# Performance work log

Hardware: AMD Instinct MI355X
Metric: run time of the kernel (lower is better)

## Reference

```python
import jax, jax.numpy as jnp
import numpy as np

N = 50000      # total nodes
NPG = 1000     # nodes per graph
B = 50         # graphs in batch
E = 800000     # positive edges
HID = 64
LN_EPS = 1e-5


def setup_inputs() -> dict:
    key = jax.random.key(0)
    ks = jax.random.split(key, 8)
    h = jax.random.normal(ks[0], (N, HID), jnp.float32)
    W1 = jax.random.normal(ks[1], (HID + 1, 2 * HID), jnp.float32) * 0.1
    b1 = jnp.zeros((2 * HID,), jnp.float32)
    ln_g = jnp.ones((2 * HID,), jnp.float32)
    ln_b = jnp.zeros((2 * HID,), jnp.float32)
    W2 = jax.random.normal(ks[2], (2 * HID, 1), jnp.float32) * 0.1
    b2 = jnp.zeros((1,), jnp.float32)
    # positive edges: endpoints within the same graph (contiguous node blocks)
    src_p = jax.random.randint(ks[3], (E,), 0, N)
    dst_p = (src_p // NPG) * NPG + jax.random.randint(ks[4], (E,), 0, NPG)
    pos_edge = jnp.stack([src_p, dst_p]).astype(jnp.int32)
    # negative edges: same-graph random pairs (stand-in for batched_negative_sampling)
    src_n = jax.random.randint(ks[5], (E,), 0, N)
    dst_n = (src_n // NPG) * NPG + jax.random.randint(ks[6], (E,), 0, NPG)
    neg_edge = jnp.stack([src_n, dst_n]).astype(jnp.int32)
    node_batch = jnp.arange(N, dtype=jnp.int32) // NPG
    return {"h": h, "W1": W1, "b1": b1, "ln_g": ln_g, "ln_b": ln_b,
            "W2": W2, "b2": b2, "pos_edge": pos_edge, "neg_edge": neg_edge,
            "node_batch": node_batch, "num_graphs": B}


def reference(h, W1, b1, ln_g, ln_b, W2, b2, pos_edge, neg_edge, node_batch, num_graphs):
    Epos = pos_edge.shape[1]
    T = 2 * Epos
    nb = int(num_graphs)
    # concat pos+neg edges, stable sort by graph id of source node
    edges_all = jnp.concatenate([pos_edge, neg_edge], axis=1)      # [2, T]
    idx = jnp.argsort(node_batch[edges_all[0]])                    # stable
    edges = edges_all[:, idx]
    conn = (idx < Epos).astype(h.dtype)                            # 1 = positive edge
    # pair features + connectivity flag -> tiny MLP score
    enc = jnp.concatenate([h[edges[0]] + h[edges[1]], conn[:, None]], axis=-1)  # [T, HID+1]
    x = enc @ W1 + b1                                              # [T, 2*HID]
    mu = jnp.mean(x, axis=-1, keepdims=True)
    var = jnp.mean((x - mu) ** 2, axis=-1, keepdims=True)
    x = (x - mu) * jax.lax.rsqrt(var + LN_EPS) * ln_g + ln_b
    x = jax.nn.relu(x)
    logits = (x @ W2)[:, 0] + b2[0]                                # [T]
    # ragged per-graph top-k: k = floor(0.9 * pos-degree count per graph)
    seg = node_batch[edges[0]]                                     # sorted segment ids
    k = jnp.floor(jax.ops.segment_sum(jnp.ones((Epos,), jnp.float32),
                                      node_batch[pos_edge[0]], num_segments=nb) * 0.9).astype(jnp.int32)
    counts = jax.ops.segment_sum(jnp.ones((T,), jnp.int32), seg, num_segments=nb)
    starts = jnp.cumsum(counts) - counts                           # segment offsets
    perm = jnp.lexsort((-logits, seg))                             # within-segment desc by logit
    seg_p = seg[perm]
    pos_in_seg = jnp.arange(T, dtype=jnp.int32) - starts[seg_p]
    mask = jnp.zeros((T,), bool).at[perm].set(pos_in_seg < k[seg_p])
    edge_weight = jnp.where(mask, logits, jnp.zeros((), logits.dtype))
    # node mask: nodes touched by any selected edge
    node_idx = edges.reshape(-1)
    vals = jnp.concatenate([mask, mask]).astype(jnp.int32)
    node_mask = jnp.zeros((h.shape[0],), jnp.int32).at[node_idx].add(vals) > 0
    return mask, edge_weight, node_mask
```

## Files before the change

### kernel.cpp

```cpp
#include <hip/hip_runtime.h>
#include <cstdint>

typedef unsigned long long u64;
typedef unsigned int u32;
typedef float f2 __attribute__((ext_vector_type(2)));

#define NGRAPH  50
#define EPOS    800000
#define TEDGE   1600000
#define HID     64
#define D2      128
#define CHUNK   1024
#define NCHUNK  1563
#define HSTRIDE 1564
#define LN_EPS  1e-5f
#define CANDCAP 4096
#define HPBLK   782
#define NBMW    1568
#define CCSTRIDE 32
#define SHSLICE 32

__device__ __forceinline__ f2 mkf2(float a, float b) { f2 r; r.x = a; r.y = b; return r; }

__device__ __forceinline__ int seg_of(int node) { return (int)((u32)node / 1000u); }

__device__ __forceinline__ u32 mapkey32(float f) {
    u32 u = __float_as_uint(f);
    return (u >> 31) ? ~u : (u | 0x80000000u);
}
__device__ __forceinline__ float unmapkey32(u32 k) {
    u32 u = (k & 0x80000000u) ? (k & 0x7FFFFFFFu) : ~k;
    return __uint_as_float(u);
}

__device__ __forceinline__ float red8(float x) {
    int t = __builtin_amdgcn_mov_dpp(__float_as_int(x), 0xB1, 0xF, 0xF, true);
    x += __int_as_float(t);
    t = __builtin_amdgcn_mov_dpp(__float_as_int(x), 0x4E, 0xF, 0xF, true);
    x += __int_as_float(t);
    t = __builtin_amdgcn_ds_swizzle(__float_as_int(x), 0x101F);
    x += __int_as_float(t);
    return x;
}

template <int NBITS>
__device__ __forceinline__ void agg_add(u32* hist, bool act, u32 bin, int lane) {
    u64 peers = __ballot(act);
#pragma unroll
    for (int b = 0; b < NBITS; ++b) {
        bool bit = (bin >> b) & 1;
        u64 bb = __ballot(act && bit);
        peers &= bit ? bb : ~bb;
    }
    if (act && (peers & ((1ull << lane) - 1ull)) == 0)
        atomicAdd(&hist[bin], (u32)__popcll(peers));
}

__device__ __forceinline__ void suffix_select(const u32* histL, u32 r, u32* wsumL,
                                              u32* selBin, u32* selRem,
                                              int tid, int lane, int wv) {
    u32 h0 = histL[2 * tid], h1 = histL[2 * tid + 1];
    u32 chunk = h0 + h1;
    u32 inc = chunk;
#pragma unroll
    for (int d = 1; d < 64; d <<= 1) {
        u32 t = __shfl_down(inc, d);
        if (lane + d < 64) inc += t;
    }
    if (lane == 0) wsumL[wv] = inc;
    __syncthreads();
    u32 S = inc;
    for (int w = wv + 1; w < 16; ++w) S += wsumL[w];
    u32 sufExcl = S - chunk;
    u32 incl1 = sufExcl + h1, incl0 = incl1 + h0;
    if (sufExcl < r && r <= incl1) { *selBin = 2 * tid + 1; *selRem = r - sufExcl; }
    else if (incl1 < r && r <= incl0) { *selBin = 2 * tid; *selRem = r - incl1; }
    __syncthreads();
}

__global__ __launch_bounds__(256) void hp_hist_kernel(const float* __restrict__ h,
                                                      const float* __restrict__ W1,
                                                      const float* __restrict__ b1,
                                                      float* __restrict__ hp,
                                                      const int* __restrict__ pos,
                                                      const int* __restrict__ neg,
                                                      int* __restrict__ histAll,
                                                      int* __restrict__ histPos) {
    __shared__ float w1s[HID * D2];
    __shared__ float hs[64 * 65];
    __shared__ int hA[NGRAPH], hP[NGRAPH];
    int bid = blockIdx.x, tid = threadIdx.x, lane = tid & 63;

    if (bid < HPBLK) {
        int n0 = bid * 64;
        for (int t = tid; t < HID * D2 / 4; t += 256)
            ((float4*)w1s)[t] = ((const float4*)W1)[t];
        for (int t = tid; t < 4096; t += 256) {
            int n = t >> 6, k = t & 63;
            int node = n0 + n;
            hs[n * 65 + k] = (node < 50000) ? h[node * HID + k] : 0.0f;
        }
        __syncthreads();
        int cg = tid & 15, ng = tid >> 4;
        int jc = cg * 8, nn = ng * 4;
        double acc[4][8];
#pragma unroll
        for (int n = 0; n < 4; ++n)
#pragma unroll
            for (int j = 0; j < 8; ++j) acc[n][j] = 0.0;
        for (int k = 0; k < HID; ++k) {
            float hv[4];
#pragma unroll
            for (int n = 0; n < 4; ++n) hv[n] = hs[(nn + n) * 65 + k];
            float4 w0 = *(const float4*)&w1s[k * D2 + jc];
            float4 w1v = *(const float4*)&w1s[k * D2 + jc + 4];
            float wf[8] = {w0.x, w0.y, w0.z, w0.w, w1v.x, w1v.y, w1v.z, w1v.w};
#pragma unroll
            for (int n = 0; n < 4; ++n)
#pragma unroll
                for (int j = 0; j < 8; ++j)
                    acc[n][j] += (double)hv[n] * (double)wf[j];
        }
        double bh[8];
#pragma unroll
        for (int j = 0; j < 8; ++j) bh[j] = 0.5 * (double)b1[jc + j];
#pragma unroll
        for (int n = 0; n < 4; ++n) {
            int node = n0 + nn + n;
            if (node < 50000) {
                float4 o0 = make_float4((float)(acc[n][0] + bh[0]), (float)(acc[n][1] + bh[1]),
                                        (float)(acc[n][2] + bh[2]), (float)(acc[n][3] + bh[3]));
                float4 o1 = make_float4((float)(acc[n][4] + bh[4]), (float)(acc[n][5] + bh[5]),
                                        (float)(acc[n][6] + bh[6]), (float)(acc[n][7] + bh[7]));
                *(float4*)&hp[node * D2 + jc] = o0;
                *(float4*)&hp[node * D2 + jc + 4] = o1;
            }
        }
    } else {
        int c = bid - HPBLK;
        if (tid < NGRAPH) { hA[tid] = 0; hP[tid] = 0; }
        __syncthreads();
        int base = c * CHUNK;
#pragma unroll
        for (int r = 0; r < 4; ++r) {
            int e = base + r * 256 + tid;
            bool valid = e < TEDGE;
            int seg = 0; bool isPos = false;
            if (valid) {
                int src = (e < EPOS) ? pos[e] : neg[e - EPOS];
                seg = seg_of(src);
                isPos = e < EPOS;
            }
            u64 peers = __ballot(valid);
#pragma unroll
            for (int b = 0; b < 6; ++b) {
                bool bit = (seg >> b) & 1;
                u64 bb = __ballot(bit);
                peers &= bit ? bb : ~bb;
            }
            u64 bpos = __ballot(isPos);
            u64 low = (1ull << lane) - 1ull;
            if (valid) {
                if ((peers & low) == 0) atomicAdd(&hA[seg], __popcll(peers));
                u64 pp = peers & bpos;
                if (isPos && (pp & low) == 0) atomicAdd(&hP[seg], __popcll(pp));
            }
        }
        __syncthreads();
        if (tid < NGRAPH) {
            histAll[tid * HSTRIDE + c] = hA[tid];
            histPos[tid * HSTRIDE + c] = hP[tid];
        }
    }
}

__global__ __launch_bounds__(1024) void scan_kernel(const int* __restrict__ histAll,
                                                    const int* __restrict__ histPos,
                                                    int* __restrict__ chunkBase,
                                                    int* __restrict__ segStart,
                                                    int* __restrict__ segCnt,
                                                    int* __restrict__ kArr) {
    __shared__ int totA[NGRAPH], totP[NGRAPH], segStartL[NGRAPH];
    int g = blockIdx.x, tid = threadIdx.x, lane = tid & 63, wv = tid >> 6;

    for (int s = wv; s < NGRAPH; s += 16) {
        int ta = 0, tp = 0;
        for (int c = lane; c < NCHUNK; c += 64) {
            ta += histAll[s * HSTRIDE + c];
            tp += histPos[s * HSTRIDE + c];
        }
        for (int m = 32; m >= 1; m >>= 1) {
            ta += __shfl_xor(ta, m);
            tp += __shfl_xor(tp, m);
        }
        if (lane == 0) { totA[s] = ta; totP[s] = tp; }
    }
    __syncthreads();
    if (tid == 0) {
        int run = 0;
        for (int s = 0; s < NGRAPH; ++s) {
            segStartL[s] = run;
            if (g == 0) {
                segStart[s] = run;
                segCnt[s] = totA[s];
                kArr[s] = (int)floorf((float)totP[s] * 0.9f);
            }
            run += totA[s];
        }
    }
    __syncthreads();
    if (wv == 0) {
        int run = segStartL[g];
        for (int b0 = 0; b0 < NCHUNK; b0 += 64) {
            int c = b0 + lane;
            int v = (c < NCHUNK) ? histAll[g * HSTRIDE + c] : 0;
            int inc = v;
            for (int d = 1; d < 64; d <<= 1) {
                int t = __shfl_up(inc, d);
                if (lane >= d) inc += t;
            }
            if (c < NCHUNK) chunkBase[g * HSTRIDE + c] = run + (inc - v);
            run += __shfl(inc, 63);
        }
    }
}

__global__ __launch_bounds__(1024) void scatter_kernel(const int* __restrict__ pos,
                                                       const int* __restrict__ neg,
                                                       const int* __restrict__ chunkBase,
                                                       int2* __restrict__ sortedE,
                                                       u32* __restrict__ selHist) {
    __shared__ int cbL[52];
    __shared__ int wcnL[16][52];
    int c = blockIdx.x, tid = threadIdx.x, lane = tid & 63, wv = tid >> 6;
    if (c < 100) selHist[c * 1024 + tid] = 0u;
    if (tid < NGRAPH) cbL[tid] = chunkBase[tid * HSTRIDE + c];
    for (int t = tid; t < 16 * 52; t += 1024) ((int*)wcnL)[t] = 0;
    __syncthreads();

    int e = c * CHUNK + tid;
    bool valid = e < TEDGE;
    int seg = 0, src = 0, dst = 0, flag = 0;
    if (valid) {
        if (e < EPOS) { src = pos[e]; dst = pos[EPOS + e]; flag = 1 << 30; }
        else          { src = neg[e - EPOS]; dst = neg[e]; flag = 0; }
        seg = seg_of(src);
    }
    u64 peers = __ballot(valid);
#pragma unroll
    for (int b = 0; b < 6; ++b) {
        bool bit = (seg >> b) & 1;
        u64 bb = __ballot(bit);
        peers &= bit ? bb : ~bb;
    }
    int intra = 0;
    if (valid) {
        u64 low = (1ull << lane) - 1ull;
        intra = __popcll(peers & low);
        if ((peers & low) == 0) wcnL[wv][seg] = __popcll(peers);
    }
    __syncthreads();
    if (tid < NGRAPH) {
        int run = cbL[tid];
#pragma unroll
        for (int w = 0; w < 16; ++w) {
            int cc = wcnL[w][tid];
            wcnL[w][tid] = run;
            run += cc;
        }
    }
    __syncthreads();
    if (valid) sortedE[wcnL[wv][seg] + intra] = make_int2(src | flag, dst);
}

#define LG_BLOCKS 6400
__global__ __launch_bounds__(256, 4) void logits_kernel(const float* __restrict__ hp,
                                                        const float* __restrict__ W1,
                                                        const float* __restrict__ lng,
                                                        const float* __restrict__ lnb,
                                                        const float* __restrict__ W2,
                                                        const float* __restrict__ b2,
                                                        const int2* __restrict__ sortedE,
                                                        u32* __restrict__ keysU) {
    int tid = threadIdx.x, wv = tid >> 6, lane = tid & 63;
    int grp = lane >> 3, q = lane & 7;
    int xcd = blockIdx.x & 7;
    int wg = (blockIdx.x >> 3) * 4 + wv;
    int edge0 = (xcd * 3200 + wg) * 64;
    if (edge0 >= TEDGE) return;

    const float4* hp4 = (const float4*)hp;
    const float4* W1r = (const float4*)(W1 + HID * D2);
    f2 wv2[8], gv2[8], ev2[8], vv2[8];
#pragma unroll
    for (int a = 0; a < 4; ++a) {
        float4 w4 = W1r[q + 8 * a];
        float4 g4 = ((const float4*)lng)[q + 8 * a];
        float4 e4 = ((const float4*)lnb)[q + 8 * a];
        float4 v4 = ((const float4*)W2)[q + 8 * a];
        wv2[2*a] = mkf2(w4.x, w4.y); wv2[2*a+1] = mkf2(w4.z, w4.w);
        gv2[2*a] = mkf2(g4.x, g4.y); gv2[2*a+1] = mkf2(g4.z, g4.w);
        ev2[2*a] = mkf2(e4.x, e4.y); ev2[2*a+1] = mkf2(e4.z, e4.w);
        vv2[2*a] = mkf2(v4.x, v4.y); vv2[2*a+1] = mkf2(v4.z, v4.w);
    }
    float bias2 = b2[0];

    int e0 = edge0 + grp;
    int2 edA = sortedE[e0];
    int2 edB = sortedE[e0 + 8];
    float4 A[4], D[4];
    {
        int src = edA.x & 0x3FFFFFFF, dst = edA.y;
#pragma unroll
        for (int a = 0; a < 4; ++a) {
            A[a] = hp4[src * 32 + q + 8 * a];
            D[a] = hp4[dst * 32 + q + 8 * a];
        }
    }

#pragma unroll
    for (int it = 0; it < 8; ++it) {
        int ecur = edge0 + it * 8 + grp;
        float connf = (float)((edA.x >> 30) & 1);
        f2 conn2 = mkf2(connf, connf);

        f2 xv[8];
#pragma unroll
        for (int a = 0; a < 4; ++a) {
            f2 alo = mkf2(A[a].x, A[a].y) + mkf2(D[a].x, D[a].y);
            f2 ahi = mkf2(A[a].z, A[a].w) + mkf2(D[a].z, D[a].w);
            xv[2*a]   = __builtin_elementwise_fma(conn2, wv2[2*a],   alo);
            xv[2*a+1] = __builtin_elementwise_fma(conn2, wv2[2*a+1], ahi);
        }

        if (it < 7) {
            int srcB = edB.x & 0x3FFFFFFF, dstB = edB.y;
#pragma unroll
            for (int a = 0; a < 4; ++a) {
                A[a] = hp4[srcB * 32 + q + 8 * a];
                D[a] = hp4[dstB * 32 + q + 8 * a];
            }
            edA = edB;
            if (it < 6) edB = sortedE[edge0 + (it + 2) * 8 + grp];
        }

        f2 s01 = xv[0] + xv[1], s23 = xv[2] + xv[3];
        f2 s45 = xv[4] + xv[5], s67 = xv[6] + xv[7];
        f2 sT = (s01 + s23) + (s45 + s67);
        f2 q0 = xv[0] * xv[0], q1 = xv[1] * xv[1], q2 = xv[2] * xv[2], q3 = xv[3] * xv[3];
        f2 q4 = xv[4] * xv[4], q5 = xv[5] * xv[5], q6 = xv[6] * xv[6], q7 = xv[7] * xv[7];
        f2 qT = ((q0 + q1) + (q2 + q3)) + ((q4 + q5) + (q6 + q7));
        float s = red8(sT.x + sT.y);
        float s2 = red8(qT.x + qT.y);
        float mu = s * 0.0078125f;
        float var = fmaf(s2, 0.0078125f, -(mu * mu)) + LN_EPS;
        float rinv = 1.0f / sqrtf(var);
        float mc = -mu * rinv;
        f2 rinv2 = mkf2(rinv, rinv), mc2 = mkf2(mc, mc), zero2 = mkf2(0.f, 0.f);

        f2 zacc = zero2;
#pragma unroll
        for (int kk = 0; kk < 8; ++kk) {
            f2 t = __builtin_elementwise_fma(xv[kk], rinv2, mc2);
            t = __builtin_elementwise_fma(t, gv2[kk], ev2[kk]);
            f2 y = __builtin_elementwise_max(t, zero2);
            zacc = __builtin_elementwise_fma(y, vv2[kk], zacc);
        }
        float z = red8(zacc.x + zacc.y);
        if (q == 0) keysU[ecur] = mapkey32(z + bias2);
    }
}

__global__ __launch_bounds__(256) void selhist_kernel(const u32* __restrict__ keysU,
                                                      const int* __restrict__ segStart,
                                                      const int* __restrict__ segCnt,
                                                      const int* __restrict__ kArr,
                                                      u32* __restrict__ selHist) {
    __shared__ u32 hb[2048];
    int bid = blockIdx.x, tid = threadIdx.x, lane = tid & 63;
    int seg = bid / SHSLICE, slice = bid % SHSLICE;
    int start = segStart[seg], cnt = segCnt[seg], k = kArr[seg];
    if (k <= 0 || k >= cnt) return;
#pragma unroll
    for (int b = 0; b < 8; ++b) hb[tid + 256 * b] = 0u;
    __syncthreads();
    int i0 = start + (int)((long long)cnt * slice / SHSLICE);
    int i1 = start + (int)((long long)cnt * (slice + 1) / SHSLICE);
    int n = i1 - i0, iters = (n + 255) >> 8;
    for (int j = 0; j < iters; ++j) {
        int i = j * 256 + tid;
        bool act = i < n;
        u32 key = act ? keysU[i0 + i] : 0u;
        agg_add<11>(hb, act, key >> 21, lane);
    }
    __syncthreads();
#pragma unroll
    for (int b = 0; b < 8; ++b) {
        u32 v = hb[tid + 256 * b];
        if (v) atomicAdd(&selHist[seg * 2048 + tid + 256 * b], v);
    }
}

__global__ __launch_bounds__(1024) void binfind_kernel(const int* __restrict__ segCnt,
                                                       const int* __restrict__ kArr,
                                                       const u32* __restrict__ selHist,
                                                       int* __restrict__ selB,
                                                       int* __restrict__ selR,
                                                       u32* __restrict__ candCnt,
                                                       u32* __restrict__ nodeBM) {
    __shared__ u32 histL[2048];
    __shared__ u32 wsumL[16];
    __shared__ u32 selBin, selRem;
    int g = blockIdx.x, tid = threadIdx.x, lane = tid & 63, wv = tid >> 6;
    int cnt = segCnt[g], k = kArr[g];
    if (tid < 32) { int w = g * 32 + tid; if (w < NBMW) nodeBM[w] = 0u; }
    u32 B; int r;
    if (k <= 0)        { B = 0xFFFFFFFFu; r = 0; }
    else if (k >= cnt) { B = 0xFFFFFFFFu; r = -1; }
    else {
        histL[tid] = selHist[g * 2048 + tid];
        histL[tid + 1024] = selHist[g * 2048 + 1024 + tid];
        __syncthreads();
        suffix_select(histL, (u32)k, wsumL, &selBin, &selRem, tid, lane, wv);
        B = selBin; r = (int)selRem;
    }
    if (tid == 0) { selB[g] = (int)B; selR[g] = r; candCnt[g * CCSTRIDE] = 0u; }
}

#define SWB ((TEDGE / 4 + 255) / 256)
__global__ __launch_bounds__(256) void segsweep_kernel(const u32* __restrict__ keysU,
                                                       const int2* __restrict__ sortedE,
                                                       const int* __restrict__ selB,
                                                       const int* __restrict__ selR,
                                                       u32* __restrict__ candCnt,
                                                       u64* __restrict__ candBuf,
                                                       u32* __restrict__ nodeBM,
                                                       float* __restrict__ outMask,
                                                       float* __restrict__ outEw) {
    __shared__ u32 bm[NBMW];
    __shared__ int sB[NGRAPH], sR[NGRAPH];
    __shared__ int segMin, segMax;
    int tid = threadIdx.x, lane = tid & 63;
    for (int t = tid; t < NBMW; t += 256) bm[t] = 0u;
    if (tid < NGRAPH) { sB[tid] = selB[tid]; sR[tid] = selR[tid]; }
    if (tid == 0) { segMin = NGRAPH - 1; segMax = 0; }
    __syncthreads();

    int e0 = (blockIdx.x * 256 + tid) * 4;
    bool act = e0 < TEDGE;
    u32 key[4]; int seg[4]; bool cand[4];
#pragma unroll
    for (int j = 0; j < 4; ++j) { seg[j] = 0; cand[j] = false; key[j] = 0u; }

    if (act) {
        uint4 kq = ((const uint4*)keysU)[e0 >> 2];
        int4 p0 = ((const int4*)sortedE)[e0 >> 1];
        int4 p1 = ((const int4*)sortedE)[(e0 >> 1) + 1];
        key[0] = kq.x; key[1] = kq.y; key[2] = kq.z; key[3] = kq.w;
        int srcA[4], dstA[4];
        srcA[0] = p0.x & 0x3FFFFFFF; dstA[0] = p0.y;
        srcA[1] = p0.z & 0x3FFFFFFF; dstA[1] = p0.w;
        srcA[2] = p1.x & 0x3FFFFFFF; dstA[2] = p1.y;
        srcA[3] = p1.z & 0x3FFFFFFF; dstA[3] = p1.w;
        float mv[4], ev[4];
#pragma unroll
        for (int j = 0; j < 4; ++j) {
            seg[j] = seg_of(srcA[j]);
            u32 B = (u32)sB[seg[j]];
            int r = sR[seg[j]];
            u32 pre = key[j] >> 21;
            bool gt = (r < 0) || (pre > B);
            cand[j] = (r > 0) && !gt && (pre == B);
            mv[j] = gt ? 1.0f : 0.0f;
            ev[j] = gt ? unmapkey32(key[j]) : 0.0f;
            if (gt) {
                atomicOr(&bm[srcA[j] >> 5], 1u << (srcA[j] & 31));
                atomicOr(&bm[dstA[j] >> 5], 1u << (dstA[j] & 31));
            }
        }
        int smin = min(min(seg[0], seg[1]), min(seg[2], seg[3]));
        int smax = max(max(seg[0], seg[1]), max(seg[2], seg[3]));
        atomicMin(&segMin, smin);
        atomicMax(&segMax, smax);
        ((float4*)outMask)[e0 >> 2] = make_float4(mv[0], mv[1], mv[2], mv[3]);
        ((float4*)outEw)[e0 >> 2]   = make_float4(ev[0], ev[1], ev[2], ev[3]);
    }

#pragma unroll
    for (int j = 0; j < 4; ++j) {
        bool c = cand[j];
        u64 bal = __ballot(c);
        while (bal) {
            int fl = (int)(__ffsll((unsigned long long)bal) - 1);
            int fg = __shfl(seg[j], fl);
            bool mine = c && (seg[j] == fg);
            u64 mm = __ballot(mine);
            u32 base = 0;
            if (lane == fl) base = atomicAdd(&candCnt[fg * CCSTRIDE], (u32)__popcll(mm));
            base = __shfl(base, fl);
            if (mine) {
                u32 p = base + (u32)__popcll(mm & ((1ull << lane) - 1ull));
                if (p < CANDCAP) candBuf[fg * CANDCAP + p] = ((u64)(~key[j]) << 32) | (u32)(e0 + j);
            }
            bal &= ~mm;
            c = c && !mine;
        }
    }
    __syncthreads();
    int w0 = (segMin * 1000) >> 5;
    int w1 = (segMax * 1000 + 999) >> 5;
    for (int w = w0 + tid; w <= w1; w += 256) {
        u32 v = bm[w];
        if (v) atomicOr(&nodeBM[w], v);
    }
}

__global__ __launch_bounds__(1024) void segfinal_kernel(const u32* __restrict__ keysU,
                                                        const int2* __restrict__ sortedE,
                                                        const int* __restrict__ segStart,
                                                        const int* __restrict__ segCnt,
                                                        const int* __restrict__ selB,
                                                        const int* __restrict__ selR,
                                                        const u32* __restrict__ candCnt,
                                                        const u64* __restrict__ candBuf,
                                                        const u32* __restrict__ nodeBM,
                                                        float* __restrict__ outMask,
                                                        float* __restrict__ outEw,
                                                        float* __restrict__ outNm) {
    __shared__ u64 arr[CANDCAP];
    __shared__ u32 histL[2048];
    __shared__ u32 wsumL[16];
    __shared__ u32 selBin, selRem;
    __shared__ int tieCnt;
    __shared__ int tieIdx[1024];
    __shared__ u32 bmw[32];
    int g = blockIdx.x, tid = threadIdx.x, lane = tid & 63, wv = tid >> 6;
    int start = segStart[g], cnt = segCnt[g];
    int segbase = g * 1000;
    int w0 = segbase >> 5;
    u32 B = (u32)selB[g]; int r = selR[g];
    if (tid < 32) bmw[tid] = nodeBM[w0 + tid];
    if (tid == 0) tieCnt = 0;
    __syncthreads();

    if (r > 0) {
        int nc = (int)candCnt[g * CCSTRIDE];
        if (nc <= CANDCAP) {
            for (int t = tid; t < nc; t += 1024) arr[t] = candBuf[g * CANDCAP + t];
            histL[tid] = 0; histL[tid + 1024] = 0;
            __syncthreads();
            int iters2 = (nc + 1023) >> 10;
            for (int j = 0; j < iters2; ++j) {
                int i = j * 1024 + tid;
                bool act = i < nc;
                u32 key = act ? ~(u32)(arr[i] >> 32) : 0u;
                agg_add<11>(histL, act, (key >> 10) & 0x7FFu, lane);
            }
            __syncthreads();
            suffix_select(histL, (u32)r, wsumL, &selBin, &selRem, tid, lane, wv);
            u32 pref2 = (B << 11) | selBin;
            u32 r2 = selRem;
            histL[tid] = 0; histL[tid + 1024] = 0;
            __syncthreads();
            for (int j = 0; j < iters2; ++j) {
                int i = j * 1024 + tid;
                bool act = i < nc;
                u32 key = act ? ~(u32)(arr[i] >> 32) : 0u;
                act = act && ((key >> 10) == pref2);
                agg_add<10>(histL, act, key & 0x3FFu, lane);
            }
            __syncthreads();
            suffix_select(histL, r2, wsumL, &selBin, &selRem, tid, lane, wv);
            u32 vKey = (pref2 << 10) | selBin;
            int m = (int)selRem;
            for (int j = 0; j < iters2; ++j) {
                int i = j * 1024 + tid;
                if (i < nc) {
                    u64 v = arr[i];
                    u32 key = ~(u32)(v >> 32);
                    int idx = (int)(u32)v;
                    if (key > vKey) {
                        outMask[idx] = 1.0f;
                        outEw[idx] = unmapkey32(key);
                        int2 ed = sortedE[idx];
                        int ns = ed.x & 0x3FFFFFFF, nd = ed.y;
                        atomicOr(&bmw[(ns >> 5) - w0], 1u << (ns & 31));
                        atomicOr(&bmw[(nd >> 5) - w0], 1u << (nd & 31));
                    } else if (key == vKey) {
                        int t = atomicAdd(&tieCnt, 1);
                        if (t < 1024) tieIdx[t] = idx;
                    }
                }
            }
            __syncthreads();
            if (wv == 0 && m > 0) {
                int t = tieCnt < 1024 ? tieCnt : 1024;
                for (int b0 = 0; b0 < t; b0 += 64) {
                    int mine = (b0 + lane < t) ? tieIdx[b0 + lane] : 0x7FFFFFFF;
                    int rank = 0;
                    for (int j = 0; j < t; ++j)
                        rank += (tieIdx[j] < mine) ? 1 : 0;
                    if (b0 + lane < t && rank < m) {
                        float vLg = unmapkey32(vKey);
                        outMask[mine] = 1.0f;
                        outEw[mine] = vLg;
                        int2 ed = sortedE[mine];
                        int ns = ed.x & 0x3FFFFFFF, nd = ed.y;
                        atomicOr(&bmw[(ns >> 5) - w0], 1u << (ns & 31));
                        atomicOr(&bmw[(nd >> 5) - w0], 1u << (nd & 31));
                    }
                }
            }
        } else {
            int iters = (cnt + 1023) >> 10;
            histL[tid] = 0; histL[tid + 1024] = 0;
            __syncthreads();
            for (int j = 0; j < iters; ++j) {
                int i = j * 1024 + tid;
                bool act = i < cnt;
                u32 key = act ? keysU[start + i] : 0u;
                act = act && ((key >> 21) == B);
                agg_add<11>(histL, act, (key >> 10) & 0x7FFu, lane);
            }
            __syncthreads();
            suffix_select(histL, (u32)r, wsumL, &selBin, &selRem, tid, lane, wv);
            u32 pref2 = (B << 11) | selBin;
            u32 r2 = selRem;
            histL[tid] = 0; histL[tid + 1024] = 0;
            __syncthreads();
            for (int j = 0; j < iters; ++j) {
                int i = j * 1024 + tid;
                bool act = i < cnt;
                u32 key = act ? keysU[start + i] : 0u;
                act = act && ((key >> 10) == pref2);
                agg_add<10>(histL, act, key & 0x3FFu, lane);
            }
            __syncthreads();
            suffix_select(histL, r2, wsumL, &selBin, &selRem, tid, lane, wv);
            u32 vKey = (pref2 << 10) | selBin;
            int m = (int)selRem;
            for (int j = 0; j < iters; ++j) {
                int i = j * 1024 + tid;
                if (i < cnt) {
                    int idx = start + i;
                    u32 key = keysU[idx];
                    if ((key >> 21) == B) {
                        if (key > vKey) {
                            outMask[idx] = 1.0f;
                            outEw[idx] = unmapkey32(key);
                            int2 ed = sortedE[idx];
                            int ns = ed.x & 0x3FFFFFFF, nd = ed.y;
                            atomicOr(&bmw[(ns >> 5) - w0], 1u << (ns & 31));
                            atomicOr(&bmw[(nd >> 5) - w0], 1u << (nd & 31));
                        } else if (key == vKey) {
                            int t = atomicAdd(&tieCnt, 1);
                            if (t < 1024) tieIdx[t] = idx;
                        }
                    }
                }
            }
            __syncthreads();
            if (wv == 0 && m > 0) {
                int t = tieCnt < 1024 ? tieCnt : 1024;
                for (int b0 = 0; b0 < t; b0 += 64) {
                    int mine = (b0 + lane < t) ? tieIdx[b0 + lane] : 0x7FFFFFFF;
                    int rank = 0;
                    for (int j = 0; j < t; ++j)
                        rank += (tieIdx[j] < mine) ? 1 : 0;
                    if (b0 + lane < t && rank < m) {
                        float vLg = unmapkey32(vKey);
                        outMask[mine] = 1.0f;
                        outEw[mine] = vLg;
                        int2 ed = sortedE[mine];
                        int ns = ed.x & 0x3FFFFFFF, nd = ed.y;
                        atomicOr(&bmw[(ns >> 5) - w0], 1u << (ns & 31));
                        atomicOr(&bmw[(nd >> 5) - w0], 1u << (nd & 31));
                    }
                }
            }
        }
    }
    __syncthreads();
    if (tid < 250) {
        int nb = tid * 4;
        float o[4];
#pragma unroll
        for (int j = 0; j < 4; ++j) {
            int node = segbase + nb + j;
            o[j] = ((bmw[(node >> 5) - w0] >> (node & 31)) & 1u) ? 1.0f : 0.0f;
        }
        ((float4*)(outNm + segbase))[tid] = make_float4(o[0], o[1], o[2], o[3]);
    }
}

extern "C" void kernel_launch(void* const* d_in, const int* in_sizes, int n_in,
                              void* d_out, int out_size, void* d_ws, size_t ws_size,
                              hipStream_t stream) {
    const float* h   = (const float*)d_in[0];
    const float* W1  = (const float*)d_in[1];
    const float* b1  = (const float*)d_in[2];
    const float* lng = (const float*)d_in[3];
    const float* lnb = (const float*)d_in[4];
    const float* W2  = (const float*)d_in[5];
    const float* b2  = (const float*)d_in[6];
    const int* pos   = (const int*)d_in[7];
    const int* neg   = (const int*)d_in[8];

    char* ws = (char*)d_ws;
    float*  hp          = (float*)(ws + 0);
    int2*   sortedE     = (int2*)(ws + 25600000);
    u32*    keysU       = (u32*)(ws + 38400000);
    int*    histAll     = (int*)(ws + 44800000);
    int*    histPos     = (int*)(ws + 45112800);
    int*    chunkBase   = (int*)(ws + 45425600);
    u32*    selHist     = (u32*)(ws + 44800000);
    int*    segStart    = (int*)(ws + 45738400);
    int*    segCnt      = (int*)(ws + 45738656);
    int*    kArr        = (int*)(ws + 45738912);
    u32*    candCnt     = (u32*)(ws + 0);
    int*    selB        = (int*)(ws + 8192);
    int*    selR        = (int*)(ws + 9216);
    u32*    nodeBM      = (u32*)(ws + 12288);
    u64*    candBuf     = (u64*)(ws + 32768);

    float* outF    = (float*)d_out;
    float* outMask = outF;
    float* outEw   = outF + TEDGE;
    float* outNm   = outF + 2 * TEDGE;

    hipLaunchKernelGGL(hp_hist_kernel, dim3(HPBLK + NCHUNK), dim3(256), 0, stream,
                       h, W1, b1, hp, pos, neg, histAll, histPos);
    hipLaunchKernelGGL(scan_kernel, dim3(NGRAPH), dim3(1024), 0, stream,
                       histAll, histPos, chunkBase, segStart, segCnt, kArr);
    hipLaunchKernelGGL(scatter_kernel, dim3(NCHUNK), dim3(1024), 0, stream,
                       pos, neg, chunkBase, sortedE, selHist);
    hipLaunchKernelGGL(logits_kernel, dim3(LG_BLOCKS), dim3(256), 0, stream,
                       hp, W1, lng, lnb, W2, b2, sortedE, keysU);
    hipLaunchKernelGGL(selhist_kernel, dim3(NGRAPH * SHSLICE), dim3(256), 0, stream,
                       keysU, segStart, segCnt, kArr, selHist);
    hipLaunchKernelGGL(binfind_kernel, dim3(NGRAPH), dim3(1024), 0, stream,
                       segCnt, kArr, selHist, selB, selR, candCnt, nodeBM);
    hipLaunchKernelGGL(segsweep_kernel, dim3(SWB), dim3(256), 0, stream,
                       keysU, sortedE, selB, selR,
                       candCnt, candBuf, nodeBM, outMask, outEw);
    hipLaunchKernelGGL(segfinal_kernel, dim3(NGRAPH), dim3(1024), 0, stream,
                       keysU, sortedE, segStart, segCnt, selB, selR,
                       candCnt, candBuf, nodeBM, outMask, outEw, outNm);
}
```

Baseline: 283.8 us.

## Fuse per-segment key histogram into logits kernel, drop selhist pass

The logits kernel now builds a block-local LDS histogram of the top 11 key bits while it computes scores. Each block then flushes the nonzero bins to the global per-segment selection histogram with atomics. A parity bit per segment lets one block span two adjacent graphs. This removes the separate selhist kernel launch and its re-read of all keys. In exchange, each block zeroes and scans a 16KB LDS histogram, which may lower occupancy, and issues many more small global atomics, including for segments the old kernel skipped.

```diff
diff --git a/kernel.cpp b/kernel.cpp
--- a/kernel.cpp
+++ b/kernel.cpp
@@ -18,7 +18,6 @@
 #define HPBLK   782
 #define NBMW    1568
 #define CCSTRIDE 32
-#define SHSLICE 32
 
 __device__ __forceinline__ f2 mkf2(float a, float b) { f2 r; r.x = a; r.y = b; return r; }
 
@@ -281,13 +280,20 @@
                                                         const float* __restrict__ W2,
                                                         const float* __restrict__ b2,
                                                         const int2* __restrict__ sortedE,
-                                                        u32* __restrict__ keysU) {
+                                                        u32* __restrict__ keysU,
+                                                        u32* __restrict__ selHist) {
+    __shared__ u32 hb[4096];
+    __shared__ int segMinS;
     int tid = threadIdx.x, wv = tid >> 6, lane = tid & 63;
     int grp = lane >> 3, q = lane & 7;
     int xcd = blockIdx.x & 7;
     int wg = (blockIdx.x >> 3) * 4 + wv;
     int edge0 = (xcd * 3200 + wg) * 64;
     if (edge0 >= TEDGE) return;
+
+    for (int t = tid; t < 4096; t += 256) hb[t] = 0u;
+    if (tid == 0) segMinS = NGRAPH;
+    __syncthreads();
 
     const float4* hp4 = (const float4*)hp;
     const float4* W1r = (const float4*)(W1 + HID * D2);
@@ -322,6 +328,7 @@
     for (int it = 0; it < 8; ++it) {
         int ecur = edge0 + it * 8 + grp;
         float connf = (float)((edA.x >> 30) & 1);
+        int curSeg = seg_of(edA.x & 0x3FFFFFFF);
         f2 conn2 = mkf2(connf, connf);
 
         f2 xv[8];
@@ -367,37 +374,23 @@
             zacc = __builtin_elementwise_fma(y, vv2[kk], zacc);
         }
         float z = red8(zacc.x + zacc.y);
-        if (q == 0) keysU[ecur] = mapkey32(z + bias2);
-    }
-}
-
-__global__ __launch_bounds__(256) void selhist_kernel(const u32* __restrict__ keysU,
-                                                      const int* __restrict__ segStart,
-                                                      const int* __restrict__ segCnt,
-                                                      const int* __restrict__ kArr,
-                                                      u32* __restrict__ selHist) {
-    __shared__ u32 hb[2048];
-    int bid = blockIdx.x, tid = threadIdx.x, lane = tid & 63;
-    int seg = bid / SHSLICE, slice = bid % SHSLICE;
-    int start = segStart[seg], cnt = segCnt[seg], k = kArr[seg];
-    if (k <= 0 || k >= cnt) return;
-#pragma unroll
-    for (int b = 0; b < 8; ++b) hb[tid + 256 * b] = 0u;
-    __syncthreads();
-    int i0 = start + (int)((long long)cnt * slice / SHSLICE);
-    int i1 = start + (int)((long long)cnt * (slice + 1) / SHSLICE);
-    int n = i1 - i0, iters = (n + 255) >> 8;
-    for (int j = 0; j < iters; ++j) {
-        int i = j * 256 + tid;
-        bool act = i < n;
-        u32 key = act ? keysU[i0 + i] : 0u;
-        agg_add<11>(hb, act, key >> 21, lane);
-    }
-    __syncthreads();
-#pragma unroll
-    for (int b = 0; b < 8; ++b) {
-        u32 v = hb[tid + 256 * b];
-        if (v) atomicAdd(&selHist[seg * 2048 + tid + 256 * b], v);
+        u32 kk32 = mapkey32(z + bias2);
+        if (q == 0) {
+            keysU[ecur] = kk32;
+            atomicMin(&segMinS, curSeg);
+        }
+        agg_add<12>(hb, q == 0, ((u32)(curSeg & 1) << 11) | (kk32 >> 21), lane);
+    }
+
+    __syncthreads();
+    int smin = segMinS;
+    for (int b = tid; b < 4096; b += 256) {
+        u32 v = hb[b];
+        if (v) {
+            int p = b >> 11;
+            int s = smin + (((smin & 1) != p) ? 1 : 0);
+            atomicAdd(&selHist[s * 2048 + (b & 2047)], v);
+        }
     }
 }
 
@@ -735,9 +728,7 @@
     hipLaunchKernelGGL(scatter_kernel, dim3(NCHUNK), dim3(1024), 0, stream,
                        pos, neg, chunkBase, sortedE, selHist);
     hipLaunchKernelGGL(logits_kernel, dim3(LG_BLOCKS), dim3(256), 0, stream,
-                       hp, W1, lng, lnb, W2, b2, sortedE, keysU);
-    hipLaunchKernelGGL(selhist_kernel, dim3(NGRAPH * SHSLICE), dim3(256), 0, stream,
-                       keysU, segStart, segCnt, kArr, selHist);
+                       hp, W1, lng, lnb, W2, b2, sortedE, keysU, selHist);
     hipLaunchKernelGGL(binfind_kernel, dim3(NGRAPH), dim3(1024), 0, stream,
                        segCnt, kArr, selHist, selB, selR, candCnt, nodeBM);
     hipLaunchKernelGGL(segsweep_kernel, dim3(SWB), dim3(256), 0, stream,
```

Measured after the change: 346.6 us. 1.22x slower.
